# Kernel tuning notes

Hardware: AMD Instinct MI355X
Metric: run time of the kernel (lower is better)

The kernel has to match this reference:

```python
import jax, jax.numpy as jnp
import numpy as np

S, B, D, H, F = 4096, 2, 512, 8, 2048
Dh = D // H
EPS = 1e-5


def _rotate_half(x):
    # matches torch: cat((-x[..., 1::2], x[..., ::2]), dim=-1)
    return jnp.concatenate([-x[..., 1::2], x[..., ::2]], axis=-1)


def _layer_norm(x, w, b):
    m = jnp.mean(x, axis=-1, keepdims=True)
    v = jnp.mean(jnp.square(x - m), axis=-1, keepdims=True)
    return (x - m) * jax.lax.rsqrt(v + EPS) * w + b


def setup_inputs() -> dict:
    key = jax.random.key(0)
    ks = jax.random.split(key, 6)
    p = lambda k, shape: (jax.random.normal(k, shape, jnp.float32) * 0.02)
    src = jax.random.normal(ks[0], (S, B, D), jnp.float32)
    # standard RoPE tables, broadcastable to [S, B, H, Dh]
    pos = jnp.arange(S, dtype=jnp.float32)
    inv_freq = 1.0 / (10000.0 ** (jnp.arange(0, Dh, 2, dtype=jnp.float32) / Dh))
    ang = pos[:, None] * inv_freq[None, :]          # [S, Dh/2]
    emb = jnp.concatenate([ang, ang], axis=-1)       # [S, Dh]
    rotary_cos = jnp.cos(emb)[:, None, None, :]
    rotary_sin = jnp.sin(emb)[:, None, None, :]
    return {
        "src": src,
        "rotary_cos": rotary_cos,
        "rotary_sin": rotary_sin,
        "in_proj_w": p(ks[1], (3 * D, D)),
        "in_proj_b": jnp.zeros((3 * D,), jnp.float32),
        "out_proj_w": p(ks[2], (D, D)),
        "out_proj_b": jnp.zeros((D,), jnp.float32),
        "w1": p(ks[3], (F, D)),
        "b1": jnp.zeros((F,), jnp.float32),
        "w2": p(ks[4], (D, F)),
        "b2": jnp.zeros((D,), jnp.float32),
        "ln1_w": jnp.ones((D,), jnp.float32),
        "ln1_b": jnp.zeros((D,), jnp.float32),
        "ln2_w": jnp.ones((D,), jnp.float32),
        "ln2_b": jnp.zeros((D,), jnp.float32),
    }


def reference(src, rotary_cos, rotary_sin, in_proj_w, in_proj_b,
              out_proj_w, out_proj_b, w1, b1, w2, b2,
              ln1_w, ln1_b, ln2_w, ln2_b):
    s = src.shape[0]
    x = _layer_norm(src, ln1_w, ln1_b)                       # [S,B,D]
    # RoPE on pre-projection tensor (q_s == k_s == x reshaped)
    xs = x.reshape(s, B, H, Dh)
    xr = (xs * rotary_cos + _rotate_half(xs) * rotary_sin).reshape(s, B, D)
    # MultiheadAttention packed in-projection
    wq, wk, wv = jnp.split(in_proj_w, 3, axis=0)
    bq, bk, bv = jnp.split(in_proj_b, 3, axis=0)
    q = (xr @ wq.T + bq).reshape(s, B, H, Dh)
    k = (xr @ wk.T + bk).reshape(s, B, H, Dh)
    v = (x @ wv.T + bv).reshape(s, B, H, Dh)
    scale = 1.0 / np.sqrt(Dh).astype(np.float32)
    scores = jnp.einsum('sbhd,tbhd->bhst', q, k) * scale     # [B,H,S,S]
    causal = jnp.triu(jnp.ones((s, s), dtype=bool), k=1)     # True = masked
    scores = jnp.where(causal, -jnp.inf, scores)
    probs = jax.nn.softmax(scores, axis=-1)
    attn = jnp.einsum('bhst,tbhd->sbhd', probs, v).reshape(s, B, D)
    attn = attn @ out_proj_w.T + out_proj_b
    src = src + attn                                         # dropout=identity (eval)
    # GELU FFN (exact erf, torch nn.GELU default)
    y = _layer_norm(src, ln2_w, ln2_b)
    y = jax.nn.gelu(y @ w1.T + b1, approximate=False) @ w2.T + b2
    return src + y
```

## Files before the change

kernel.cpp:

```cpp
#include <hip/hip_runtime.h>
#include <hip/hip_bf16.h>

typedef unsigned short u16;
typedef unsigned int u32;
using short8 = __attribute__((ext_vector_type(8))) short;
using f32x4  = __attribute__((ext_vector_type(4))) float;
using f32x16 = __attribute__((ext_vector_type(16))) float;

#define MFMA16(a,b,c) __builtin_amdgcn_mfma_f32_16x16x32_bf16((a),(b),(c),0,0,0)
#define MFMA32(a,b,c) __builtin_amdgcn_mfma_f32_32x32x16_bf16((a),(b),(c),0,0,0)
#define EXP2F(x) __builtin_amdgcn_exp2f(x)

__device__ __forceinline__ float bf2f(u16 u){
  union { u32 i; float f; } v; v.i = ((u32)u)<<16; return v.f;
}
__device__ __forceinline__ u16 f2bf(float f){
  u32 x = __float_as_uint(f);
  x += 0x7fffu + ((x>>16)&1u);
  return (u16)(x>>16);
}
__device__ __forceinline__ u32 cvtpk(float lo, float hi){
  u32 r;
  asm("v_cvt_pk_bf16_f32 %0, %1, %2" : "=v"(r) : "v"(lo), "v"(hi));
  return r;
}
__device__ __forceinline__ float cross_max(float v){
  u32 b = __float_as_uint(v);
  auto r = __builtin_amdgcn_permlane32_swap(b, b, false, false);
  return fmaxf(__uint_as_float(r[0]), __uint_as_float(r[1]));
}
__device__ __forceinline__ float cross_sum(float v){
  u32 b = __float_as_uint(v);
  auto r = __builtin_amdgcn_permlane32_swap(b, b, false, false);
  return __uint_as_float(r[0]) + __uint_as_float(r[1]);
}

typedef __attribute__((address_space(1))) const u32 GU32;
typedef __attribute__((address_space(3))) u32 LU32;
typedef __attribute__((address_space(3))) const u16 LDSU16C;
__device__ __forceinline__ void gload_lds16(const void* g, void* l){
  __builtin_amdgcn_global_load_lds((GU32*)g, (LU32*)l, 16, 0, 0);
}

template<int OFF>
__device__ __forceinline__ uint2 tr16(const u16* p){
  uint2 r;
  if constexpr (OFF == 0)
    asm volatile("ds_read_b64_tr_b16 %0, %1" : "=v"(r) : "v"((LDSU16C*)p));
  else
    asm volatile("ds_read_b64_tr_b16 %0, %1 offset:128" : "=v"(r) : "v"((LDSU16C*)p));
  return r;
}

struct ConvArgs {
  const float4* in[14];
  uint2* out[14];
  int n4[14];
  int sb[15];
};
__global__ __launch_bounds__(256)
void conv_all(ConvArgs a)
{
  int bid = blockIdx.x;
  int s = 0;
  while (s < 13 && bid >= a.sb[s+1]) ++s;
  int i = (bid - a.sb[s])*256 + threadIdx.x;
  if (i >= a.n4[s]) return;
  float4 v = a.in[s][i];
  union { uint2 u; u16 h[4]; } o;
  o.h[0] = f2bf(v.x); o.h[1] = f2bf(v.y);
  o.h[2] = f2bf(v.z); o.h[3] = f2bf(v.w);
  a.out[s][i] = o.u;
}

template<int DO_ROPE, int IN_F32>
__global__ __launch_bounds__(256)
void ln_kernel(const void* __restrict__ inv, const u16* __restrict__ lw,
               const u16* __restrict__ lb, const u16* __restrict__ ct,
               const u16* __restrict__ st, u16* __restrict__ xo,
               u16* __restrict__ xro)
{
  __shared__ float xs[4][512];
  int tid = threadIdx.x, wid = tid>>6, lane = tid&63;
  int m = blockIdx.x*4 + wid;
  int d0 = lane*8;
  float v[8], sum = 0.f, sq = 0.f;
  if (IN_F32){
    const float* in = (const float*)inv;
    float4 a = *(const float4*)(in + (size_t)m*512 + d0);
    float4 b = *(const float4*)(in + (size_t)m*512 + d0 + 4);
    v[0]=a.x; v[1]=a.y; v[2]=a.z; v[3]=a.w;
    v[4]=b.x; v[5]=b.y; v[6]=b.z; v[7]=b.w;
  } else {
    const u16* in = (const u16*)inv;
    union { uint4 q; u16 s[8]; } pk;
    pk.q = *(const uint4*)(in + (size_t)m*512 + d0);
#pragma unroll
    for (int j=0;j<8;j++) v[j] = bf2f(pk.s[j]);
  }
#pragma unroll
  for (int j=0;j<8;j++){ sum+=v[j]; sq+=v[j]*v[j]; }
#pragma unroll
  for (int o=1;o<64;o<<=1){ sum += __shfl_xor(sum,o); sq += __shfl_xor(sq,o); }
  float mean = sum*(1.f/512.f);
  float var  = sq*(1.f/512.f) - mean*mean;
  float rstd = rsqrtf(var + 1e-5f);
  float xn[8];
  union { uint4 q; u16 s[8]; } ou;
#pragma unroll
  for (int j=0;j<8;j++){
    int d = d0+j;
    xn[j] = (v[j]-mean)*rstd*bf2f(lw[d]) + bf2f(lb[d]);
    ou.s[j] = f2bf(xn[j]);
  }
  *(uint4*)(xo + (size_t)m*512 + d0) = ou.q;
  if (DO_ROPE){
#pragma unroll
    for (int j=0;j<8;j++) xs[wid][d0+j] = xn[j];
    __syncthreads();
    int si = m>>1;
    int hb = d0 & ~63;
#pragma unroll
    for (int j=0;j<8;j++){
      int d = d0+j, jh = d&63;
      float rh = (jh<32) ? -xs[wid][hb + 2*jh+1] : xs[wid][hb + 2*(jh-32)];
      float c  = bf2f(ct[si*64+jh]);
      float s2 = bf2f(st[si*64+jh]);
      ou.s[j] = f2bf(xn[j]*c + rh*s2);
    }
    *(uint4*)(xro + (size_t)m*512 + d0) = ou.q;
  }
}

#define EPI_NONE 0
#define EPI_GELU 1
#define EPI_RES  2

template<int EPI, int RES_F32, int OUT_F32, int QSCL, int SELA, int BM>
__global__ __launch_bounds__(256)
void gemm_bt(const u16* __restrict__ A, const u16* __restrict__ W,
             const u16* __restrict__ bias, const void* __restrict__ resv,
             void* __restrict__ Cv, int M, int N, int K)
{
  constexpr int IF = BM/32;
  __shared__ u16 As[BM*32];
  __shared__ u16 Bs[128*32];
  int tid = threadIdx.x, wid = tid>>6, lane = tid&63;
  int l15 = lane & 15, g4 = lane >> 4;
  int nbn = N >> 7;
  int bm = blockIdx.x / nbn, bn = blockIdx.x % nbn;
  int wr = wid >> 1, wc = wid & 1;
  f32x4 acc[IF][4];
#pragma unroll
  for (int i=0;i<IF;i++)
#pragma unroll
    for (int j=0;j<4;j++) acc[i][j] = (f32x4){0.f,0.f,0.f,0.f};

  const u16* Ap = (SELA && bn >= 8) ? (const u16*)resv : A;
  const u16* Abase = Ap + (size_t)(bm*BM)*K;
  const u16* Wbase = W + (size_t)(bn*128)*K;
  int rowB = wid*32 + (lane>>2);
  int colA = (lane&3)*8;

  for (int kb = 0; kb < K; kb += 32){
    if constexpr (BM == 128){
#pragma unroll
      for (int j=0;j<2;j++)
        gload_lds16(Abase + (size_t)(rowB + j*16)*K + kb + colA, &As[(wid*32 + j*16)*32]);
    } else {
      int rowA = wid*16 + (lane>>2);
      gload_lds16(Abase + (size_t)rowA*K + kb + colA, &As[wid*16*32]);
    }
#pragma unroll
    for (int j=0;j<2;j++)
      gload_lds16(Wbase + (size_t)(rowB + j*16)*K + kb + colA, &Bs[(wid*32 + j*16)*32]);
    __syncthreads();
    short8 af[IF], bf8[4];
    int ro = 8*g4;
#pragma unroll
    for (int i=0;i<IF;i++)
      af[i]  = *(const short8*)&As[(wr*(16*IF) + i*16 + l15)*32 + ro];
#pragma unroll
    for (int j=0;j<4;j++)
      bf8[j] = *(const short8*)&Bs[(wc*64 + j*16 + l15)*32 + ro];
#pragma unroll
    for (int i=0;i<IF;i++)
#pragma unroll
      for (int j=0;j<4;j++)
        acc[i][j] = MFMA16(af[i], bf8[j], acc[i][j]);
    __syncthreads();
  }
  int r0 = bm*BM + wr*(16*IF) + 4*g4;
  int c0 = bn*128 + wc*64 + l15;
#pragma unroll
  for (int i=0;i<IF;i++){
#pragma unroll
    for (int j=0;j<4;j++){
      int col = c0 + j*16;
      float bv = bf2f(bias[col]);
#pragma unroll
      for (int r=0;r<4;r++){
        int row = r0 + i*16 + r;
        size_t idx = (size_t)row*N + col;
        float x = acc[i][j][r] + bv;
        if (EPI == EPI_GELU) x = 0.5f*x*(1.f + erff(x*0.70710678118f));
        if (EPI == EPI_RES){
          if (RES_F32) x += ((const float*)resv)[idx];
          else         x += bf2f(((const u16*)resv)[idx]);
        }
        if (QSCL && col < 512) x *= 0.18033688011f;
        if (OUT_F32) ((float*)Cv)[idx] = x;
        else         ((u16*)Cv)[idx]   = f2bf(x);
      }
    }
  }
}

__global__ __launch_bounds__(256, 3)
void attn_kernel(const u16* __restrict__ QKV, u16* __restrict__ Opart,
                 float* __restrict__ ml, u16* __restrict__ O)
{
  __shared__ u16 Ks[2][64*64];
  __shared__ u16 Vp[2][4*1024];
  int tid = threadIdx.x, wid = tid>>6, lane = tid&63;
  int l15 = lane&15, q5 = lane&31, hi = lane>>5;
  int bid = blockIdx.x;
  int qt, kt0, kt1, cid = bid;
  bool split = (bid < 768);
  if (split){
    int idx = bid >> 4;
    qt = 31 - (idx >> 1);
    int half = idx & 1;
    int nk = 2*qt + 2, h0 = nk >> 1;
    kt0 = half ? h0 : 0; kt1 = half ? nk : h0;
  } else {
    qt = 7 - ((bid - 768) >> 4);
    kt0 = 0; kt1 = 2*qt + 2;
  }
  int bh = bid & 15;
  int b = bh>>3, h = bh&7;
  size_t qkvb = (size_t)b*1536 + h*64;
  size_t vbh  = (size_t)b*512  + h*64;

  int qrow = qt*128 + wid*32 + q5;
  short8 aQ[4];
#pragma unroll
  for (int kc=0; kc<4; ++kc)
    aQ[kc] = *(const short8*)(QKV + (size_t)qrow*3072 + qkvb + 16*kc + 8*hi);

  f32x16 oacc[2];
#pragma unroll
  for (int dblk=0; dblk<2; ++dblk)
#pragma unroll
    for (int r=0;r<16;r++) oacc[dblk][r] = 0.f;
  float mrun = -3e38f, lrun = 0.f;

#define STAGE(KT, BUF)                                                              \
  {                                                                                 \
    _Pragma("unroll")                                                               \
    for (int i=0;i<2;++i){                                                          \
      gload_lds16(QKV + (size_t)((KT)*64 + wid*16 + i*8 + (lane>>3))*3072 + qkvb    \
                      + 512 + (((lane&7)^(lane>>3))<<3),                            \
                  &Ks[BUF][(wid*16 + i*8)*64]);                                     \
      int j = wid*2 + i, p = j>>1, rh = (j&1)*32;                                   \
      gload_lds16(QKV + (size_t)((KT)*64 + rh + (lane>>1))*3072 + qkvb              \
                      + 1024 + p*16 + ((lane&1)<<3),                                \
                  &Vp[BUF][p*1024 + rh*16]);                                        \
    }                                                                               \
  }

  STAGE(kt0, 0);
  int cur = 0;

  for (int kt=kt0; kt<kt1; ++kt){
    __syncthreads();
    if (kt+1 < kt1) STAGE(kt+1, cur^1);

    f32x16 sacc[2];
#pragma unroll
    for (int s=0;s<2;s++)
#pragma unroll
      for (int r=0;r<16;r++) sacc[s][r] = 0.f;
#pragma unroll
    for (int kc=0; kc<4; ++kc)
#pragma unroll
      for (int s=0; s<2; ++s){
        int cb = (32*kc + 16*hi) ^ ((q5&7)<<4);
        short8 aK = *(const short8*)&Ks[cur][(32*s + q5)*64 + (cb>>1)];
        sacc[s] = MFMA32(aK, aQ[kc], sacc[s]);
      }

    uint2 av[4][2][2];
#pragma unroll
    for (int kc=0; kc<4; ++kc)
#pragma unroll
      for (int dblk=0; dblk<2; ++dblk){
        const u16* base = &Vp[cur][(((lane>>4)&1) + 2*dblk)*1024 + (16*kc + 8*hi)*16 + l15*4];
        av[kc][dblk][0] = tr16<0>(base);
        av[kc][dblk][1] = tr16<128>(base);
      }

    bool diag = (kt >= 2*qt);
    float pm[4] = {-3e38f,-3e38f,-3e38f,-3e38f};
#pragma unroll
    for (int s=0;s<2;++s)
#pragma unroll
      for (int r=0;r<16;++r){
        float x = sacc[s][r];
        if (diag){
          int kv = kt*64 + 32*s + (r&3) + 8*(r>>2) + 4*hi;
          if (kv > qrow) x = -3e38f;
          sacc[s][r] = x;
        }
        pm[r&3] = fmaxf(pm[r&3], x);
      }
    float pmax = fmaxf(fmaxf(pm[0],pm[1]), fmaxf(pm[2],pm[3]));
    pmax = cross_max(pmax);
    if (!__all(pmax <= mrun + 8.f)){
      float mn = fmaxf(mrun, pmax);
      float alpha = EXP2F(mrun - mn);
      mrun = mn;
      lrun *= alpha;
#pragma unroll
      for (int dblk=0; dblk<2; ++dblk)
#pragma unroll
        for (int r=0;r<16;++r) oacc[dblk][r] *= alpha;
    }
    float ps = 0.f;
    u32 Wp[2][4][2];
#pragma unroll
    for (int s=0;s<2;++s)
#pragma unroll
      for (int p=0;p<4;++p){
        float e0 = EXP2F(sacc[s][4*p+0]-mrun);
        float e1 = EXP2F(sacc[s][4*p+1]-mrun);
        float e2 = EXP2F(sacc[s][4*p+2]-mrun);
        float e3 = EXP2F(sacc[s][4*p+3]-mrun);
        ps += (e0+e1)+(e2+e3);
        Wp[s][p][0] = cvtpk(e0,e1);
        Wp[s][p][1] = cvtpk(e2,e3);
      }
    ps = cross_sum(ps);
    lrun += ps;

    asm volatile("s_waitcnt lgkmcnt(0)");
    __builtin_amdgcn_sched_barrier(0);
#pragma unroll
    for (int kc=0; kc<4; ++kc){
      int s = kc>>1, pA = (2*kc)&3, pB = (2*kc+1)&3;
      auto r0 = __builtin_amdgcn_permlane32_swap(Wp[s][pA][0], Wp[s][pB][0], false, false);
      auto r1 = __builtin_amdgcn_permlane32_swap(Wp[s][pA][1], Wp[s][pB][1], false, false);
      union { u32 w[4]; short8 s8; } bp;
      bp.w[0]=r0[0]; bp.w[1]=r1[0]; bp.w[2]=r0[1]; bp.w[3]=r1[1];
      union { uint2 u2[2]; short8 s8; } a0, a1;
      a0.u2[0]=av[kc][0][0]; a0.u2[1]=av[kc][0][1];
      a1.u2[0]=av[kc][1][0]; a1.u2[1]=av[kc][1][1];
      oacc[0] = MFMA32(a0.s8, bp.s8, oacc[0]);
      oacc[1] = MFMA32(a1.s8, bp.s8, oacc[1]);
    }
    cur ^= 1;
  }

  if (split){
    u16* po = Opart + (size_t)cid*8192 + (wid*32 + q5)*64;
#pragma unroll
    for (int dblk=0; dblk<2; ++dblk)
#pragma unroll
      for (int p=0;p<4;++p){
        int d0 = 32*dblk + 8*p + 4*hi;
        union { uint2 u; u16 hh[4]; } o;
#pragma unroll
        for (int r=0;r<4;++r) o.hh[r] = f2bf(oacc[dblk][4*p+r]);
        *(uint2*)(po + d0) = o.u;
      }
    if (lane < 32){
      ml[((size_t)cid*128 + wid*32 + q5)*2 + 0] = mrun;
      ml[((size_t)cid*128 + wid*32 + q5)*2 + 1] = lrun;
    }
  } else {
    float rcp = 1.f / lrun;
#pragma unroll
    for (int dblk=0; dblk<2; ++dblk)
#pragma unroll
      for (int p=0;p<4;++p){
        int d0 = 32*dblk + 8*p + 4*hi;
        union { uint2 u; u16 hh[4]; } o;
#pragma unroll
        for (int r=0;r<4;++r) o.hh[r] = f2bf(oacc[dblk][4*p+r] * rcp);
        *(uint2*)(O + (size_t)qrow*1024 + vbh + d0) = o.u;
      }
  }
#undef STAGE
}

__global__ __launch_bounds__(128)
void attn_combine(const u16* __restrict__ Opart, const float* __restrict__ ml,
                  u16* __restrict__ O)
{
  int cb = blockIdx.x >> 4;
  int qt = 31 - cb;
  int bh = blockIdx.x & 15;
  int b = bh>>3, h = bh&7;
  int q = threadIdx.x;
  int cid0 = (cb*2)*16 + bh, cid1 = cid0 + 16;
  float m0 = ml[((size_t)cid0*128 + q)*2], l0 = ml[((size_t)cid0*128 + q)*2 + 1];
  float m1 = ml[((size_t)cid1*128 + q)*2], l1 = ml[((size_t)cid1*128 + q)*2 + 1];
  float mx = fmaxf(m0, m1);
  float w0 = EXP2F(m0 - mx), w1 = EXP2F(m1 - mx);
  float rcp = 1.f / (w0*l0 + w1*l1);
  w0 *= rcp; w1 *= rcp;
  const u16* p0 = Opart + ((size_t)cid0*128 + q)*64;
  const u16* p1 = Opart + ((size_t)cid1*128 + q)*64;
  u16* o = O + (size_t)(qt*128 + q)*1024 + b*512 + h*64;
#pragma unroll
  for (int d0=0; d0<64; d0+=8){
    union { uint4 v; u16 s[8]; } a, c, r;
    a.v = *(const uint4*)(p0 + d0);
    c.v = *(const uint4*)(p1 + d0);
#pragma unroll
    for (int j=0;j<8;j++) r.s[j] = f2bf(w0*bf2f(a.s[j]) + w1*bf2f(c.s[j]));
    *(uint4*)(o + d0) = r.v;
  }
}

extern "C" void kernel_launch(void* const* d_in, const int* in_sizes, int n_in,
                              void* d_out, int out_size, void* d_ws, size_t ws_size,
                              hipStream_t stream)
{
  float* out = (float*)d_out;
  const float* src_f = (const float*)d_in[0];
  char* ws = (char*)d_ws;
  const size_t MB = 1024ull*1024ull;
  u16* xbuf = (u16*)(ws);
  u16* xr   = (u16*)(ws +  8*MB);
  u16* qkv  = (u16*)(ws + 16*MB);
  u16* y2   = (u16*)(ws + 16*MB);
  u16* hb   = (u16*)(ws + 24*MB);
  u16* opart= (u16*)(ws + 40*MB);
  float* mlb= (float*)(ws + 52*MB);
  u16* arena= (u16*)(ws + 56*MB);
  u16* attn = xbuf;
  u16* src2 = xr;

  ConvArgs ca;
  u16* cv[15]; cv[0] = nullptr;
  {
    size_t off = 0; int blk = 0;
    for (int i=1;i<15;i++){
      cv[i] = arena + off;
      int n = in_sizes[i];
      ca.in[i-1]  = (const float4*)d_in[i];
      ca.out[i-1] = (uint2*)cv[i];
      ca.n4[i-1]  = n >> 2;
      ca.sb[i-1]  = blk;
      blk += ((n>>2) + 255) / 256;
      off += (size_t)n;
    }
    ca.sb[14] = blk;
    conv_all<<<blk, 256, 0, stream>>>(ca);
  }
  const u16* rcos = cv[1];
  const u16* rsin = cv[2];
  const u16* inw  = cv[3];
  const u16* inb  = cv[4];
  const u16* outw = cv[5];
  const u16* outb = cv[6];
  const u16* w1   = cv[7];
  const u16* b1   = cv[8];
  const u16* w2   = cv[9];
  const u16* b2   = cv[10];
  const u16* ln1w = cv[11];
  const u16* ln1b = cv[12];
  const u16* ln2w = cv[13];
  const u16* ln2b = cv[14];

  ln_kernel<1,1><<<2048, 256, 0, stream>>>(src_f, ln1w, ln1b, rcos, rsin, xbuf, xr);

  gemm_bt<EPI_NONE,0,0,1,1,128><<<768, 256, 0, stream>>>(xr, inw, inb, xbuf, qkv, 8192, 1536, 512);

  attn_kernel<<<896, 256, 0, stream>>>(qkv, opart, mlb, attn);
  attn_combine<<<384, 128, 0, stream>>>(opart, mlb, attn);

  gemm_bt<EPI_RES,1,0,0,0,64><<<512, 256, 0, stream>>>(attn, outw, outb, src_f, src2, 8192, 512, 512);

  ln_kernel<0,0><<<2048, 256, 0, stream>>>(src2, ln2w, ln2b, nullptr, nullptr, y2, nullptr);

  gemm_bt<EPI_GELU,0,0,0,0,128><<<1024, 256, 0, stream>>>(y2, w1, b1, nullptr, hb, 8192, 2048, 512);
  gemm_bt<EPI_RES,0,1,0,0,64><<<512, 256, 0, stream>>>(hb, w2, b2, src2, out, 8192, 512, 2048);
}
```

Baseline: 210.3 us.

## Widen GEMM K-tile to 64 with XOR-swizzled LDS, add attention MFMA priority

The GEMM main loop now stages 64-wide K slices instead of 32. LDS tiles are doubled and XOR-swizzled on both the global-to-LDS store and the fragment reads to avoid bank conflicts. This halves the number of barrier pairs per K and issues two MFMA sub-steps per stage, at the cost of more LDS per block. The attention kernel also raises wave priority around its QK and PV MFMA blocks to favour matrix-core issue over other waves.

```diff
diff --git a/kernel.cpp b/kernel.cpp
--- a/kernel.cpp
+++ b/kernel.cpp
@@ -143,8 +143,8 @@
              void* __restrict__ Cv, int M, int N, int K)
 {
   constexpr int IF = BM/32;
-  __shared__ u16 As[BM*32];
-  __shared__ u16 Bs[128*32];
+  __shared__ u16 As[BM*64];
+  __shared__ u16 Bs[128*64];
   int tid = threadIdx.x, wid = tid>>6, lane = tid&63;
   int l15 = lane & 15, g4 = lane >> 4;
   int nbn = N >> 7;
@@ -159,35 +159,38 @@
   const u16* Ap = (SELA && bn >= 8) ? (const u16*)resv : A;
   const u16* Abase = Ap + (size_t)(bm*BM)*K;
   const u16* Wbase = W + (size_t)(bn*128)*K;
-  int rowB = wid*32 + (lane>>2);
-  int colA = (lane&3)*8;
-
-  for (int kb = 0; kb < K; kb += 32){
-    if constexpr (BM == 128){
-#pragma unroll
-      for (int j=0;j<2;j++)
-        gload_lds16(Abase + (size_t)(rowB + j*16)*K + kb + colA, &As[(wid*32 + j*16)*32]);
-    } else {
-      int rowA = wid*16 + (lane>>2);
-      gload_lds16(Abase + (size_t)rowA*K + kb + colA, &As[wid*16*32]);
-    }
-#pragma unroll
-    for (int j=0;j<2;j++)
-      gload_lds16(Wbase + (size_t)(rowB + j*16)*K + kb + colA, &Bs[(wid*32 + j*16)*32]);
+  int srow = lane>>3;
+  int schk = ((lane&7) ^ srow) << 3;
+  int swz  = (l15 & 7) << 3;
+
+  for (int kb = 0; kb < K; kb += 64){
+#pragma unroll
+    for (int i=0;i<IF;i++){
+      int row = wid*(8*IF) + i*8 + srow;
+      gload_lds16(Abase + (size_t)row*K + kb + schk, &As[(wid*(8*IF) + i*8)*64]);
+    }
+#pragma unroll
+    for (int i=0;i<4;i++){
+      int row = wid*32 + i*8 + srow;
+      gload_lds16(Wbase + (size_t)row*K + kb + schk, &Bs[(wid*32 + i*8)*64]);
+    }
     __syncthreads();
-    short8 af[IF], bf8[4];
-    int ro = 8*g4;
-#pragma unroll
-    for (int i=0;i<IF;i++)
-      af[i]  = *(const short8*)&As[(wr*(16*IF) + i*16 + l15)*32 + ro];
-#pragma unroll
-    for (int j=0;j<4;j++)
-      bf8[j] = *(const short8*)&Bs[(wc*64 + j*16 + l15)*32 + ro];
-#pragma unroll
-    for (int i=0;i<IF;i++)
+#pragma unroll
+    for (int ks=0; ks<2; ++ks){
+      short8 af[IF], bf8[4];
+      int co = 32*ks + 8*g4;
+#pragma unroll
+      for (int i=0;i<IF;i++)
+        af[i]  = *(const short8*)&As[(wr*(16*IF) + i*16 + l15)*64 + (co ^ swz)];
 #pragma unroll
       for (int j=0;j<4;j++)
-        acc[i][j] = MFMA16(af[i], bf8[j], acc[i][j]);
+        bf8[j] = *(const short8*)&Bs[(wc*64 + j*16 + l15)*64 + (co ^ swz)];
+#pragma unroll
+      for (int i=0;i<IF;i++)
+#pragma unroll
+        for (int j=0;j<4;j++)
+          acc[i][j] = MFMA16(af[i], bf8[j], acc[i][j]);
+    }
     __syncthreads();
   }
   int r0 = bm*BM + wr*(16*IF) + 4*g4;
@@ -281,6 +284,7 @@
     for (int s=0;s<2;s++)
 #pragma unroll
       for (int r=0;r<16;r++) sacc[s][r] = 0.f;
+    __builtin_amdgcn_s_setprio(1);
 #pragma unroll
     for (int kc=0; kc<4; ++kc)
 #pragma unroll
@@ -289,6 +293,7 @@
         short8 aK = *(const short8*)&Ks[cur][(32*s + q5)*64 + (cb>>1)];
         sacc[s] = MFMA32(aK, aQ[kc], sacc[s]);
       }
+    __builtin_amdgcn_s_setprio(0);
 
     uint2 av[4][2][2];
 #pragma unroll
@@ -345,6 +350,7 @@
 
     asm volatile("s_waitcnt lgkmcnt(0)");
     __builtin_amdgcn_sched_barrier(0);
+    __builtin_amdgcn_s_setprio(1);
 #pragma unroll
     for (int kc=0; kc<4; ++kc){
       int s = kc>>1, pA = (2*kc)&3, pB = (2*kc+1)&3;
@@ -358,6 +364,7 @@
       oacc[0] = MFMA32(a0.s8, bp.s8, oacc[0]);
       oacc[1] = MFMA32(a1.s8, bp.s8, oacc[1]);
     }
+    __builtin_amdgcn_s_setprio(0);
     cur ^= 1;
   }
 
```

New measurement: 201.5 us. 1.04x faster.
